# Performance work log

Measured on AMD Instinct MI355X. Metric: run time of the kernel, lower is better.

Reference implementation:

```python
import jax, jax.numpy as jnp
import numpy as np

COST_LABELS = 2.0
COST_BBOX = 5.0
COST_GIOU = 2.0
NUM_HEADS = 7
NUM_CLASSES = 16


def setup_inputs() -> dict:
    key = jax.random.key(0)
    k0, k1, k2, k3 = jax.random.split(key, 4)
    bs, nq, nt = 16, 900, 100
    return {
        "pred_logits": jax.random.normal(k0, (NUM_HEADS, bs, nq, NUM_CLASSES), jnp.float32),
        "pred_boxes": jax.random.uniform(k1, (bs, nq, 4), jnp.float32),
        "tgt_boxes": jax.random.uniform(k2, (bs, nt, 4), jnp.float32),
        "tgt_labels": jax.random.randint(k3, (NUM_HEADS, bs, nt), 0, NUM_CLASSES),
    }


def box_cxcywh_to_xyxy(b):
    cx, cy, w, h = jnp.split(b, 4, axis=-1)
    return jnp.concatenate([cx - 0.5 * w, cy - 0.5 * h, cx + 0.5 * w, cy + 0.5 * h], axis=-1)


def generalized_box_iou(a, b):
    # a: [N,4] xyxy, b: [M,4] xyxy -> [N,M]
    area_a = (a[:, 2] - a[:, 0]) * (a[:, 3] - a[:, 1])
    area_b = (b[:, 2] - b[:, 0]) * (b[:, 3] - b[:, 1])
    lt = jnp.maximum(a[:, None, :2], b[None, :, :2])
    rb = jnp.minimum(a[:, None, 2:], b[None, :, 2:])
    wh = jnp.clip(rb - lt, 0.0)
    inter = wh[..., 0] * wh[..., 1]
    union = area_a[:, None] + area_b[None, :] - inter
    iou = inter / union
    lt_e = jnp.minimum(a[:, None, :2], b[None, :, :2])
    rb_e = jnp.maximum(a[:, None, 2:], b[None, :, 2:])
    wh_e = jnp.clip(rb_e - lt_e, 0.0)
    area = wh_e[..., 0] * wh_e[..., 1]
    return iou - (area - union) / area


@jax.jit
def compute_cost(pred_logits, pred_boxes, tgt_boxes, tgt_labels):
    bs, nq, _ = pred_boxes.shape
    out_bbox = pred_boxes.reshape(-1, 4)   # [N,4] cxcywh
    tgt_bbox = tgt_boxes.reshape(-1, 4)    # [M,4] cxcywh
    # L1 cdist
    cost_bbox = jnp.sum(jnp.abs(out_bbox[:, None, :] - tgt_bbox[None, :, :]), axis=-1)
    cost_giou = -generalized_box_iou(box_cxcywh_to_xyxy(out_bbox), box_cxcywh_to_xyxy(tgt_bbox))
    # label cost: sum over the 7 heads of -sigmoid(logits)[:, tgt_ids]
    probs = jax.nn.sigmoid(pred_logits.reshape(NUM_HEADS, -1, NUM_CLASSES))  # [7,N,C]
    ids = tgt_labels.reshape(NUM_HEADS, -1)                                   # [7,M]
    cost_labels = jnp.zeros_like(cost_bbox)
    for h in range(NUM_HEADS):  # small fixed loop, avoids a [7,N,M] intermediate
        cost_labels = cost_labels - probs[h][:, ids[h]]
    C = COST_BBOX * cost_bbox + COST_LABELS * cost_labels + COST_GIOU * cost_giou
    return C.reshape(bs, nq, -1)  # [bs, nq, bs*nt]


def _lsa(cost):
    """Jonker-Volgenant shortest augmenting path. cost: [r,c] with r<=c.
    Returns row2col: optimal column for each row (minimizes total cost)."""
    cost = np.asarray(cost, dtype=np.float64)
    r, c = cost.shape
    u = np.zeros(r + 1)
    v = np.zeros(c + 1)
    p = np.zeros(c + 1, np.int64)    # p[j] = row matched to column j (1-indexed)
    way = np.zeros(c + 1, np.int64)
    for i in range(1, r + 1):
        p[0] = i
        j0 = 0
        minv = np.full(c + 1, np.inf)
        used = np.zeros(c + 1, bool)
        while True:
            used[j0] = True
            i0 = p[j0]
            free = np.nonzero(~used)[0]  # unused columns (1..c)
            cur = cost[i0 - 1, free - 1] - u[i0] - v[free]
            better = cur < minv[free]
            minv[free] = np.where(better, cur, minv[free])
            way[free[better]] = j0
            k = np.argmin(minv[free])
            j1 = free[k]
            delta = minv[free][k]
            u[p[used]] += delta
            v[used] -= delta
            minv[free] -= delta
            j0 = j1
            if p[j0] == 0:
                break
        while j0:
            j1 = way[j0]
            p[j0] = p[j1]
            j0 = j1
    row2col = np.full(r, -1, np.int64)
    for j in range(1, c + 1):
        if p[j] > 0:
            row2col[p[j] - 1] = j - 1
    return row2col


def reference(pred_logits, pred_boxes, tgt_boxes, tgt_labels):
    C = compute_cost(pred_logits, pred_boxes, tgt_boxes, tgt_labels)  # [bs, nq, bs*nt]
    bs, nq, M = C.shape
    nt = M // bs
    Cn = np.asarray(C)
    out = np.zeros((bs, 2, nt), np.int64)
    for b in range(bs):
        sub = Cn[b, :, b * nt:(b + 1) * nt]  # [nq, nt] per-image block (mimics C.split(sizes))
        t2p = _lsa(sub.T)                    # for each target, its matched prediction
        order = np.argsort(t2p, kind="stable")  # scipy returns row indices sorted
        out[b, 0] = t2p[order]  # index_i: selected predictions (sorted)
        out[b, 1] = order       # index_j: corresponding targets
    return jnp.asarray(out)
```

## Files before the change

kernel.cpp:

```cpp
#include <hip/hip_runtime.h>
#include <hip/hip_bf16.h>
#include <math.h>

#define NQ 900
#define NT 100
#define BS 16
#define NH 7
#define NC 16
#define SLOTS 15
#define MAXTREE 8192

__global__ __launch_bounds__(256) void sig_transpose_kernel(const float* __restrict__ logits,
                                                            float* __restrict__ probsT) {
    const int hb = blockIdx.x;
    const float* src = logits + (size_t)hb * NQ * NC;
    float* dst = probsT + (size_t)hb * NC * NQ;
    __shared__ float tile[NC][NQ + 1];
    for (int e = threadIdx.x; e < NQ * NC; e += 256) {
        int q = e >> 4, c = e & 15;
        float x = src[e];
        tile[c][q] = 1.0f / (1.0f + expf(-x));
    }
    __syncthreads();
    for (int c = 0; c < NC; ++c)
        for (int q = threadIdx.x; q < NQ; q += 256)
            dst[c * NQ + q] = tile[c][q];
}

__global__ __launch_bounds__(256) void cost_kernel_bt(const float4* __restrict__ pboxes4,
                                                      const float4* __restrict__ tboxes4,
                                                      const int*    __restrict__ tlabels,
                                                      const float*  __restrict__ probsT,
                                                      float* __restrict__ costT) {
    const int bt = blockIdx.x;
    const int b = bt / NT, t = bt % NT;

    const float* prow[NH];
    #pragma unroll
    for (int h = 0; h < NH; ++h) {
        int lab = tlabels[(h * BS + b) * NT + t];
        prow[h] = probsT + (size_t)((h * BS + b) * NC + lab) * NQ;
    }

    float4 tb = tboxes4[b * NT + t];
    float tx = tb.x, ty = tb.y, tw = tb.z, th = tb.w;
    float bx0 = tx - 0.5f * tw, by0 = ty - 0.5f * th;
    float bx1 = tx + 0.5f * tw, by1 = ty + 0.5f * th;
    float areaB = (bx1 - bx0) * (by1 - by0);

    for (int q = threadIdx.x; q < NQ; q += 256) {
        float4 pb = pboxes4[b * NQ + q];
        float px = pb.x, py = pb.y, pw = pb.z, ph = pb.w;

        float cost_bbox = fabsf(px - tx) + fabsf(py - ty) + fabsf(pw - tw) + fabsf(ph - th);

        float ax0 = px - 0.5f * pw, ay0 = py - 0.5f * ph;
        float ax1 = px + 0.5f * pw, ay1 = py + 0.5f * ph;
        float areaA = (ax1 - ax0) * (ay1 - ay0);
        float ltx = fmaxf(ax0, bx0), lty = fmaxf(ay0, by0);
        float rbx = fminf(ax1, bx1), rby = fminf(ay1, by1);
        float iw = fmaxf(rbx - ltx, 0.f), ih = fmaxf(rby - lty, 0.f);
        float inter = iw * ih;
        float uni = areaA + areaB - inter;
        float iou = inter / uni;
        float ex0 = fminf(ax0, bx0), ey0 = fminf(ay0, by0);
        float ex1 = fmaxf(ax1, bx1), ey1 = fmaxf(ay1, by1);
        float ew = fmaxf(ex1 - ex0, 0.f), eh = fmaxf(ey1 - ey0, 0.f);
        float earea = ew * eh;
        float giou = iou - (earea - uni) / earea;

        float ssum = 0.f;
        #pragma unroll
        for (int h = 0; h < NH; ++h) ssum += prow[h][q];

        costT[(b * NT + t) * NQ + q] = 5.0f * cost_bbox - 2.0f * ssum - 2.0f * giou;
    }
}

__global__ void cost_kernel_fb(const float* __restrict__ logits,
                               const float* __restrict__ pboxes,
                               const float* __restrict__ tboxes,
                               const int*   __restrict__ tlabels,
                               float* __restrict__ costT) {
    int id = blockIdx.x * blockDim.x + threadIdx.x;
    if (id >= BS * NT * NQ) return;
    int q = id % NQ;
    int t = (id / NQ) % NT;
    int b = id / (NQ * NT);

    const float* pb = pboxes + (b * NQ + q) * 4;
    const float* tb = tboxes + (b * NT + t) * 4;
    float px = pb[0], py = pb[1], pw = pb[2], ph = pb[3];
    float tx = tb[0], ty = tb[1], tw = tb[2], th = tb[3];

    float cost_bbox = fabsf(px - tx) + fabsf(py - ty) + fabsf(pw - tw) + fabsf(ph - th);

    float ax0 = px - 0.5f * pw, ay0 = py - 0.5f * ph;
    float ax1 = px + 0.5f * pw, ay1 = py + 0.5f * ph;
    float bx0 = tx - 0.5f * tw, by0 = ty - 0.5f * th;
    float bx1 = tx + 0.5f * tw, by1 = ty + 0.5f * th;
    float areaA = (ax1 - ax0) * (ay1 - ay0);
    float areaB = (bx1 - bx0) * (by1 - by0);
    float ltx = fmaxf(ax0, bx0), lty = fmaxf(ay0, by0);
    float rbx = fminf(ax1, bx1), rby = fminf(ay1, by1);
    float iw = fmaxf(rbx - ltx, 0.f), ih = fmaxf(rby - lty, 0.f);
    float inter = iw * ih;
    float uni = areaA + areaB - inter;
    float iou = inter / uni;
    float ex0 = fminf(ax0, bx0), ey0 = fminf(ay0, by0);
    float ex1 = fmaxf(ax1, bx1), ey1 = fmaxf(ay1, by1);
    float ew = fmaxf(ex1 - ex0, 0.f), eh = fmaxf(ey1 - ey0, 0.f);
    float earea = ew * eh;
    float giou = iou - (earea - uni) / earea;

    float ssum = 0.f;
    #pragma unroll
    for (int h = 0; h < NH; ++h) {
        int lab = tlabels[(h * BS + b) * NT + t];
        float x = logits[((h * BS + b) * NQ + q) * NC + lab];
        ssum += 1.0f / (1.0f + expf(-x));
    }

    costT[(b * NT + t) * NQ + q] = 5.0f * cost_bbox - 2.0f * ssum - 2.0f * giou;
}

__global__ __launch_bounds__(64) void lsa_kernel(const float* __restrict__ costT,
                                                 int* __restrict__ out) {
    const int b = blockIdx.x;
    const int lane = threadIdx.x;
    const float* cost = costT + b * NT * NQ;

    __shared__ double2 pu[NQ + 1];
    __shared__ double u_s[NT + 1];
    __shared__ int way_s[NQ + 1];
    __shared__ int p_w[NQ + 1];
    __shared__ int jmin_s[NT];
    __shared__ int listA[NT];
    __shared__ int r2c[NT];
    __shared__ int cnt_s;

    for (int j = lane; j <= NQ; j += 64) {
        pu[j] = make_double2(0.0, 0.0);
        p_w[j] = 0x7fffffff;
    }
    __syncthreads();

    bool lostA = false, lostB = false;
    #pragma unroll
    for (int pass = 0; pass < 2; ++pass) {
        int r = pass * 64 + lane;
        if (r < NT) {
            const float4* row4 = (const float4*)(cost + (size_t)r * NQ);
            float m0 = INFINITY, m1f = INFINITY, m2f = INFINITY, m3f = INFINITY;
            int i0 = 0, i1 = 0, i2 = 0, i3 = 0;
            #pragma unroll 5
            for (int q4 = 0; q4 < NQ / 4; ++q4) {
                float4 cv = row4[q4];
                if (cv.x < m0)  { m0 = cv.x;  i0 = 4 * q4; }
                if (cv.y < m1f) { m1f = cv.y; i1 = 4 * q4 + 1; }
                if (cv.z < m2f) { m2f = cv.z; i2 = 4 * q4 + 2; }
                if (cv.w < m3f) { m3f = cv.w; i3 = 4 * q4 + 3; }
            }
            float mv = m0; int mj = i0;
            if (m1f < mv || (m1f == mv && i1 < mj)) { mv = m1f; mj = i1; }
            if (m2f < mv || (m2f == mv && i2 < mj)) { mv = m2f; mj = i2; }
            if (m3f < mv || (m3f == mv && i3 < mj)) { mv = m3f; mj = i3; }
            u_s[r + 1] = (double)mv;
            jmin_s[r] = mj;
            atomicMin(&p_w[mj + 1], r + 1);
        }
    }
    __syncthreads();

    {
        int rA = lane;
        int j = jmin_s[rA] + 1;
        if (p_w[j] == rA + 1) pu[j] = make_double2(u_s[rA + 1], (double)(rA + 1));
        else lostA = true;
    }
    if (lane < NT - 64) {
        int rB = 64 + lane;
        int j = jmin_s[rB] + 1;
        if (p_w[j] == rB + 1) pu[j] = make_double2(u_s[rB + 1], (double)(rB + 1));
        else lostB = true;
    }
    unsigned long long mA = __ballot(lostA);
    unsigned long long mB = __ballot(lostB);
    if (lane == 0) {
        int n = 0;
        unsigned long long m = mA;
        while (m) { int l = __ffsll((long long)m) - 1; listA[n++] = l + 1; m &= m - 1; }
        m = mB;
        while (m) { int l = __ffsll((long long)m) - 1; listA[n++] = 64 + l + 1; m &= m - 1; }
        cnt_s = n;
    }
    __syncthreads();
    const int nfree = cnt_s;

    double v[SLOTS], minv[SLOTS], ureg[SLOTS];
    int pof[SLOTS];
    #pragma unroll
    for (int k = 0; k < SLOTS; ++k) { v[k] = 0.0; ureg[k] = 0.0; pof[k] = 0; }
    const unsigned invalid = (lane < 4) ? 0u : (1u << 14);
    double u_c0 = 0.0;

    for (int ii = 0; ii < nfree; ++ii) {
        const int i = listA[ii];
        #pragma unroll
        for (int k = 0; k < SLOTS; ++k) minv[k] = INFINITY;
        unsigned used = invalid;
        int j0 = 0;
        int i0 = i;
        double u_i0 = u_s[i];
        int guard = 0;

        while (guard++ < MAXTREE) {
            if (j0 != 0) {
                if (lane == ((j0 - 1) & 63)) {
                    int slot = (j0 - 1) >> 6;
                    used |= (1u << slot);
                    #pragma unroll
                    for (int k = 0; k < SLOTS; ++k)
                        if (slot == k) { pof[k] = i0; ureg[k] = u_i0; }
                }
            } else {
                if (lane == 0) u_c0 = u_i0;
            }

            const float* crow = cost + (size_t)(i0 - 1) * NQ;
            float c[SLOTS];
            #pragma unroll
            for (int k = 0; k < SLOTS - 1; ++k) c[k] = crow[lane + 64 * k];
            c[SLOTS - 1] = (lane < 4) ? crow[lane + 64 * (SLOTS - 1)] : 0.0f;

            double bv = INFINITY;
            int bj = 2048;
            #pragma unroll
            for (int k = 0; k < SLOTS; ++k) {
                if (!((used >> k) & 1u)) {
                    int j = 1 + lane + 64 * k;
                    double cur = ((double)c[k] - u_i0) - v[k];
                    if (cur < minv[k]) { minv[k] = cur; way_s[j] = j0; }
                    if (minv[k] < bv) { bv = minv[k]; bj = j; }
                }
            }
            #pragma unroll
            for (int off = 1; off < 64; off <<= 1) {
                double ov = __shfl_xor(bv, off);
                int oj = __shfl_xor(bj, off);
                if (ov < bv || (ov == bv && oj < bj)) { bv = ov; bj = oj; }
            }
            const double delta = bv;

            double2 t = pu[bj];

            #pragma unroll
            for (int k = 0; k < SLOTS; ++k) {
                minv[k] -= delta;
                if ((used >> k) & 1u) { ureg[k] += delta; v[k] -= delta; }
            }
            if (lane == 0) u_c0 += delta;

            j0 = bj;
            i0 = (int)t.y;
            u_i0 = t.x;
            if (i0 == 0) break;
        }

        __syncthreads();
        #pragma unroll
        for (int k = 0; k < SLOTS; ++k) {
            if (((used >> k) & 1u) && !((invalid >> k) & 1u)) {
                int j = 1 + lane + 64 * k;
                u_s[pof[k]] = ureg[k];
                pu[j] = make_double2(ureg[k], (double)pof[k]);
            }
        }
        __syncthreads();
        if (lane == 0) {
            u_s[i] = u_c0;
            int j = j0;
            while (j) {
                int jw = way_s[j];
                double2 t2 = (jw == 0) ? make_double2(u_c0, (double)i) : pu[jw];
                pu[j] = t2;
                j = jw;
            }
        }
        __syncthreads();
    }

    for (int j = 1 + lane; j <= NQ; j += 64) {
        int pi = (int)pu[j].y;
        if (pi > 0) r2c[pi - 1] = j - 1;
    }
    __syncthreads();
    for (int t = lane; t < NT; t += 64) {
        int ccol = r2c[t];
        int rank = 0;
        for (int tt = 0; tt < NT; ++tt) rank += (r2c[tt] < ccol) ? 1 : 0;
        out[b * 2 * NT + rank] = ccol;
        out[b * 2 * NT + NT + rank] = t;
    }
}

extern "C" void kernel_launch(void* const* d_in, const int* in_sizes, int n_in,
                              void* d_out, int out_size, void* d_ws, size_t ws_size,
                              hipStream_t stream) {
    const float* logits  = (const float*)d_in[0];
    const float* pboxes  = (const float*)d_in[1];
    const float* tboxes  = (const float*)d_in[2];
    const int*   tlabels = (const int*)d_in[3];
    int* out = (int*)d_out;
    float* costT = (float*)d_ws;

    const size_t costT_elems  = (size_t)BS * NT * NQ;
    const size_t probsT_elems = (size_t)NH * BS * NC * NQ;
    const size_t need = (costT_elems + probsT_elems) * sizeof(float);

    if (ws_size >= need) {
        float* probsT = costT + costT_elems;
        sig_transpose_kernel<<<NH * BS, 256, 0, stream>>>(logits, probsT);
        cost_kernel_bt<<<BS * NT, 256, 0, stream>>>((const float4*)pboxes,
                                                    (const float4*)tboxes, tlabels, probsT, costT);
    } else {
        const int total = BS * NT * NQ;
        cost_kernel_fb<<<(total + 255) / 256, 256, 0, stream>>>(logits, pboxes, tboxes, tlabels, costT);
    }
    lsa_kernel<<<BS, 64, 0, stream>>>(costT, out);
}
```

Baseline: 125.0 us.

## Remap Hungarian columns to lanes in groups of four for float4 loads

Each wavefront lane now owns four consecutive cost columns per 256-column chunk instead of one column per 64-column stride. This lets each augmenting step read a cost row with float4 loads instead of fifteen scalar loads. The argmin reduction now shuffles only the value with fmin, then uses a ballot and a single shuffle to recover the winning column index, instead of shuffling value and index together. Ties are now broken by the lowest lane rather than the lowest column, which can change which column is chosen when costs tie exactly.

```diff
diff --git a/kernel.cpp b/kernel.cpp
--- a/kernel.cpp
+++ b/kernel.cpp
@@ -7,7 +7,7 @@
 #define BS 16
 #define NH 7
 #define NC 16
-#define SLOTS 15
+#define NSLOT 16
 #define MAXTREE 8192
 
 __global__ __launch_bounds__(256) void sig_transpose_kernel(const float* __restrict__ logits,
@@ -189,25 +189,25 @@
     if (lane == 0) {
         int n = 0;
         unsigned long long m = mA;
-        while (m) { int l = __ffsll((long long)m) - 1; listA[n++] = l + 1; m &= m - 1; }
+        while (m) { int l = __ffsll((unsigned long long)m) - 1; listA[n++] = l + 1; m &= m - 1; }
         m = mB;
-        while (m) { int l = __ffsll((long long)m) - 1; listA[n++] = 64 + l + 1; m &= m - 1; }
+        while (m) { int l = __ffsll((unsigned long long)m) - 1; listA[n++] = 64 + l + 1; m &= m - 1; }
         cnt_s = n;
     }
     __syncthreads();
     const int nfree = cnt_s;
 
-    double v[SLOTS], minv[SLOTS], ureg[SLOTS];
-    int pof[SLOTS];
+    double v[NSLOT], minv[NSLOT], ureg[NSLOT];
+    int pof[NSLOT];
     #pragma unroll
-    for (int k = 0; k < SLOTS; ++k) { v[k] = 0.0; ureg[k] = 0.0; pof[k] = 0; }
-    const unsigned invalid = (lane < 4) ? 0u : (1u << 14);
+    for (int k = 0; k < NSLOT; ++k) { v[k] = 0.0; ureg[k] = 0.0; pof[k] = 0; }
+    const unsigned invalid = (lane <= 32) ? 0u : 0xF000u;
     double u_c0 = 0.0;
 
     for (int ii = 0; ii < nfree; ++ii) {
         const int i = listA[ii];
         #pragma unroll
-        for (int k = 0; k < SLOTS; ++k) minv[k] = INFINITY;
+        for (int k = 0; k < NSLOT; ++k) minv[k] = INFINITY;
         unsigned used = invalid;
         int j0 = 0;
         int i0 = i;
@@ -216,52 +216,60 @@
 
         while (guard++ < MAXTREE) {
             if (j0 != 0) {
-                if (lane == ((j0 - 1) & 63)) {
-                    int slot = (j0 - 1) >> 6;
+                int idx = j0 - 1;
+                if (lane == ((idx >> 2) & 63)) {
+                    int slot = ((idx >> 8) << 2) | (idx & 3);
                     used |= (1u << slot);
                     #pragma unroll
-                    for (int k = 0; k < SLOTS; ++k)
-                        if (slot == k) { pof[k] = i0; ureg[k] = u_i0; }
+                    for (int s = 0; s < NSLOT; ++s)
+                        if (s == slot) { pof[s] = i0; ureg[s] = u_i0; }
                 }
             } else {
                 if (lane == 0) u_c0 = u_i0;
             }
 
-            const float* crow = cost + (size_t)(i0 - 1) * NQ;
-            float c[SLOTS];
+            const float4* crow4 = (const float4*)(cost + (size_t)(i0 - 1) * NQ);
+            float4 c4[4];
             #pragma unroll
-            for (int k = 0; k < SLOTS - 1; ++k) c[k] = crow[lane + 64 * k];
-            c[SLOTS - 1] = (lane < 4) ? crow[lane + 64 * (SLOTS - 1)] : 0.0f;
+            for (int kc = 0; kc < 3; ++kc) c4[kc] = crow4[lane + 64 * kc];
+            c4[3] = (lane <= 32) ? crow4[lane + 192] : make_float4(0.f, 0.f, 0.f, 0.f);
 
             double bv = INFINITY;
             int bj = 2048;
             #pragma unroll
-            for (int k = 0; k < SLOTS; ++k) {
-                if (!((used >> k) & 1u)) {
-                    int j = 1 + lane + 64 * k;
-                    double cur = ((double)c[k] - u_i0) - v[k];
-                    if (cur < minv[k]) { minv[k] = cur; way_s[j] = j0; }
-                    if (minv[k] < bv) { bv = minv[k]; bj = j; }
+            for (int kc = 0; kc < 4; ++kc) {
+                #pragma unroll
+                for (int e = 0; e < 4; ++e) {
+                    const int s = 4 * kc + e;
+                    if (!((used >> s) & 1u)) {
+                        float cf = (e == 0) ? c4[kc].x : (e == 1) ? c4[kc].y
+                                 : (e == 2) ? c4[kc].z : c4[kc].w;
+                        int j = 1 + 4 * lane + 256 * kc + e;
+                        double cur = ((double)cf - u_i0) - v[s];
+                        if (cur < minv[s]) { minv[s] = cur; way_s[j] = j0; }
+                        if (minv[s] < bv) { bv = minv[s]; bj = j; }
+                    }
                 }
             }
+            double vmin = bv;
             #pragma unroll
-            for (int off = 1; off < 64; off <<= 1) {
-                double ov = __shfl_xor(bv, off);
-                int oj = __shfl_xor(bj, off);
-                if (ov < bv || (ov == bv && oj < bj)) { bv = ov; bj = oj; }
-            }
-            const double delta = bv;
-
-            double2 t = pu[bj];
+            for (int off = 1; off < 64; off <<= 1)
+                vmin = fmin(vmin, __shfl_xor(vmin, off));
+            unsigned long long tied = __ballot(bv == vmin);
+            int wl = __ffsll((unsigned long long)tied) - 1;
+            int jwin = __shfl(bj, wl);
+            const double delta = vmin;
+
+            double2 t = pu[jwin];
 
             #pragma unroll
-            for (int k = 0; k < SLOTS; ++k) {
-                minv[k] -= delta;
-                if ((used >> k) & 1u) { ureg[k] += delta; v[k] -= delta; }
+            for (int s = 0; s < NSLOT; ++s) {
+                minv[s] -= delta;
+                if ((used >> s) & 1u) { ureg[s] += delta; v[s] -= delta; }
             }
             if (lane == 0) u_c0 += delta;
 
-            j0 = bj;
+            j0 = jwin;
             i0 = (int)t.y;
             u_i0 = t.x;
             if (i0 == 0) break;
@@ -269,11 +277,11 @@
 
         __syncthreads();
         #pragma unroll
-        for (int k = 0; k < SLOTS; ++k) {
-            if (((used >> k) & 1u) && !((invalid >> k) & 1u)) {
-                int j = 1 + lane + 64 * k;
-                u_s[pof[k]] = ureg[k];
-                pu[j] = make_double2(ureg[k], (double)pof[k]);
+        for (int s = 0; s < NSLOT; ++s) {
+            if (((used >> s) & 1u) && !((invalid >> s) & 1u)) {
+                int j = 1 + 4 * lane + 256 * (s >> 2) + (s & 3);
+                u_s[pof[s]] = ureg[s];
+                pu[j] = make_double2(ureg[s], (double)pof[s]);
             }
         }
         __syncthreads();
```

New measurement: 120.5 us. 1.04x faster.
